# Kernel optimization log

Hardware: AMD Instinct MI355X
Metric: run time of the kernel (lower is better)

The kernel has to match this reference:

```python
import jax, jax.numpy as jnp
import numpy as np

N = 200000
E = 600000
C = 256


def setup_inputs() -> dict:
    key = jax.random.key(0)
    k1, k2, k3, k4, k5 = jax.random.split(key, 5)
    x = jax.random.normal(k1, (N, C), dtype=jnp.float32)
    sources = jax.random.randint(k2, (E,), 0, N, dtype=jnp.int64)
    targets = jax.random.randint(k3, (E,), 0, N, dtype=jnp.int64)
    norm = jax.random.uniform(k4, (N, 1), dtype=jnp.float32)
    # xavier_normal for [C, C]: std = sqrt(2 / (fan_in + fan_out))
    std = float(np.sqrt(2.0 / (C + C)))
    weight = jax.random.normal(k5, (C, C), dtype=jnp.float32) * std
    return {"x": x, "sources": sources, "targets": targets, "norm": norm, "weight": weight}


def reference(x, sources, targets, norm, weight):
    # out-of-place index_add: x + scatter_add(x[sources] -> targets)
    agg = x.at[targets].add(x[sources])  # [N, C]
    h = norm * agg                        # [N, C], norm broadcasts over channels
    return h @ weight                     # [N, C]
```

## Files before the change

kernel.cpp:

```cpp
#include <hip/hip_runtime.h>
#include <hip/hip_bf16.h>

#define NN 200000
#define NE 600000
#define CH 256
#define NBLK_SCAN 196
#define ZW_GRID 512
#define ZW_TILES 6250

typedef short bf16x8 __attribute__((ext_vector_type(8)));
typedef float f32x4 __attribute__((ext_vector_type(4)));
typedef unsigned short ushort8v __attribute__((ext_vector_type(8)));

__device__ __forceinline__ unsigned short f2bf(float f) {
    unsigned int u = __builtin_bit_cast(unsigned int, f);
    u = (u + 0x7FFFu + ((u >> 16) & 1u)) >> 16;
    return (unsigned short)u;
}
__device__ __forceinline__ float bf2f(unsigned short u) {
    unsigned int v = ((unsigned int)u) << 16;
    return __builtin_bit_cast(float, v);
}

__global__ void k_wt(const float* __restrict__ W, unsigned short* __restrict__ Wt) {
    int j = blockIdx.x, k = threadIdx.x;
    Wt[j * CH + k] = f2bf(W[k * CH + j]);
}

__global__ __launch_bounds__(256) void k_prep(const float* __restrict__ W,
                                              unsigned short* __restrict__ Wt,
                                              const int* __restrict__ te,
                                              int* __restrict__ deg) {
    const int t = blockIdx.x * 256 + threadIdx.x;
    const int S = gridDim.x * 256;
    for (int e = t; e < NE; e += S) atomicAdd(&deg[te[e]], 1);
    for (int i = t; i < CH * CH; i += S) {
        int j = i >> 8, k = i & 255;
        Wt[j * CH + k] = f2bf(W[k * CH + j]);
    }
}

__global__ __launch_bounds__(256) void k_scanA(const int* __restrict__ deg,
                                               int* __restrict__ off,
                                               int* __restrict__ bsum) {
    __shared__ int ts[256];
    int tid = threadIdx.x;
    int base = blockIdx.x * 1024 + tid * 4;
    int v[4];
#pragma unroll
    for (int j = 0; j < 4; ++j) {
        int idx = base + j;
        v[j] = (idx < NN) ? deg[idx] : 0;
    }
    int tsum = v[0] + v[1] + v[2] + v[3];
    ts[tid] = tsum;
    __syncthreads();
    int x = tsum;
    for (int ofs = 1; ofs < 256; ofs <<= 1) {
        int y = (tid >= ofs) ? ts[tid - ofs] : 0;
        __syncthreads();
        x += y;
        ts[tid] = x;
        __syncthreads();
    }
    int run = x - tsum;
#pragma unroll
    for (int j = 0; j < 4; ++j) {
        int idx = base + j;
        if (idx < NN) off[idx] = run;
        run += v[j];
    }
    if (tid == 255) bsum[blockIdx.x] = x;
}

__global__ __launch_bounds__(256) void k_scanC(int* __restrict__ off,
                                               const int* __restrict__ bsum,
                                               int* __restrict__ cur) {
    __shared__ int ts[256];
    int tid = threadIdx.x;
    int v = (tid < NBLK_SCAN) ? bsum[tid] : 0;
    ts[tid] = v;
    __syncthreads();
    int x = v;
    for (int ofs = 1; ofs < 256; ofs <<= 1) {
        int y = (tid >= ofs) ? ts[tid - ofs] : 0;
        __syncthreads();
        x += y;
        ts[tid] = x;
        __syncthreads();
    }
    const int bo = (blockIdx.x == 0) ? 0 : ts[blockIdx.x - 1];
    int base = blockIdx.x * 1024 + tid * 4;
#pragma unroll
    for (int j = 0; j < 4; ++j) {
        int idx = base + j;
        if (idx < NN) {
            int o = off[idx] + bo;
            off[idx] = o;
            cur[idx] = o;
        }
    }
}

__global__ void k_fill(const int* __restrict__ se, const int* __restrict__ te,
                       int* __restrict__ cur, int* __restrict__ elist) {
    int e = blockIdx.x * 256 + threadIdx.x;
    if (e < NE) {
        int t = te[e];
        int pos = atomicAdd(&cur[t], 1);
        elist[pos] = se[e];
    }
}

__global__ __launch_bounds__(256, 2) void k_zw(const float* __restrict__ x,
                                               const unsigned short* __restrict__ Wt,
                                               unsigned short* __restrict__ zbf,
                                               const int* __restrict__ te,
                                               int* __restrict__ deg) {
    __shared__ float lds[2][32 * CH];
    const int tid = threadIdx.x;
    const int wid = tid >> 6;
    const int lane = tid & 63;
    const int r16 = lane & 15;
    const int q = lane >> 4;

#define STAGE(buf, tile)                                                                  \
    {                                                                                     \
        const float* src = x + (size_t)(tile) * 32 * CH;                                  \
        _Pragma("unroll")                                                                 \
        for (int i = 0; i < 8; ++i) {                                                     \
            const int fi = i * 1024 + tid * 4;                                            \
            const int row = fi >> 8;                                                      \
            const int g = (fi & 255) >> 2;                                                \
            const int sg = g ^ (row & 7);                                                 \
            __builtin_amdgcn_global_load_lds(                                             \
                (const __attribute__((address_space(1))) void*)(src + row * CH + sg * 4), \
                (__attribute__((address_space(3))) void*)(&lds[buf][fi]), 16, 0, 0);      \
        }                                                                                 \
    }

    int t = blockIdx.x;
    STAGE(0, t)

    bf16x8 breg[8][4];
    {
        const unsigned short* wb = Wt + (size_t)(wid * 64 + r16) * CH + q * 8;
#pragma unroll
        for (int kk = 0; kk < 8; ++kk)
#pragma unroll
            for (int nt = 0; nt < 4; ++nt)
                breg[kk][nt] = *reinterpret_cast<const bf16x8*>(wb + (size_t)nt * 16 * CH + kk * 32);
    }

    for (int e = blockIdx.x * 256 + tid; e < NE; e += ZW_GRID * 256)
        atomicAdd(&deg[te[e]], 1);

    int cur = 0;
    for (; t < ZW_TILES; t += ZW_GRID) {
        const int tn = t + ZW_GRID;
        if (tn < ZW_TILES) STAGE(cur ^ 1, tn)
        __syncthreads();

        f32x4 acc[2][4];
#pragma unroll
        for (int m = 0; m < 2; ++m)
#pragma unroll
            for (int nt = 0; nt < 4; ++nt) acc[m][nt] = (f32x4){0.f, 0.f, 0.f, 0.f};

#pragma unroll
        for (int kk = 0; kk < 8; ++kk) {
            bf16x8 a[2];
#pragma unroll
            for (int m = 0; m < 2; ++m) {
                const int lr = m * 16 + r16;
                const int sw = lr & 7;
                const float* lp = &lds[cur][lr * CH];
                const int g0 = kk * 8 + q * 2;
                f32x4 lo = *reinterpret_cast<const f32x4*>(lp + ((g0 ^ sw) << 2));
                f32x4 hi = *reinterpret_cast<const f32x4*>(lp + (((g0 + 1) ^ sw) << 2));
                a[m][0] = (short)f2bf(lo[0]); a[m][1] = (short)f2bf(lo[1]);
                a[m][2] = (short)f2bf(lo[2]); a[m][3] = (short)f2bf(lo[3]);
                a[m][4] = (short)f2bf(hi[0]); a[m][5] = (short)f2bf(hi[1]);
                a[m][6] = (short)f2bf(hi[2]); a[m][7] = (short)f2bf(hi[3]);
            }
#pragma unroll
            for (int m = 0; m < 2; ++m)
#pragma unroll
                for (int nt = 0; nt < 4; ++nt)
                    acc[m][nt] = __builtin_amdgcn_mfma_f32_16x16x32_bf16(a[m], breg[kk][nt], acc[m][nt], 0, 0, 0);
        }

        const int rb = t * 32;
#pragma unroll
        for (int m = 0; m < 2; ++m) {
#pragma unroll
            for (int nt = 0; nt < 4; ++nt) {
                unsigned short* po = zbf + (size_t)(rb + m * 16 + q * 4) * CH
                                   + wid * 64 + nt * 16 + r16;
#pragma unroll
                for (int r = 0; r < 4; ++r) po[(size_t)r * CH] = f2bf(acc[m][nt][r]);
            }
        }
        __syncthreads();
        cur ^= 1;
    }
#undef STAGE
}

__global__ __launch_bounds__(256) void k_gout(const unsigned short* __restrict__ zbf,
                                              const int* __restrict__ off,
                                              const int* __restrict__ deg,
                                              const int* __restrict__ elist,
                                              const float* __restrict__ norm,
                                              float* __restrict__ out) {
    int wid = threadIdx.x >> 6;
    int lane = threadIdx.x & 63;
    int row = blockIdx.x * 4 + wid;
    if (row >= NN) return;
    int start = off[row];
    int d = deg[row];
    const int uo = lane * 4;
    ushort4 bv = *reinterpret_cast<const ushort4*>(zbf + (size_t)row * CH + uo);
    float ax = bf2f(bv.x), ay = bf2f(bv.y), az = bf2f(bv.z), aw = bf2f(bv.w);
    int e = 0;
    while (e < d) {
        int i0 = (e + 0 < d) ? elist[start + e + 0] : -1;
        int i1 = (e + 1 < d) ? elist[start + e + 1] : -1;
        int i2 = (e + 2 < d) ? elist[start + e + 2] : -1;
        int i3 = (e + 3 < d) ? elist[start + e + 3] : -1;
        int i4 = (e + 4 < d) ? elist[start + e + 4] : -1;
        int i5 = (e + 5 < d) ? elist[start + e + 5] : -1;
        int i6 = (e + 6 < d) ? elist[start + e + 6] : -1;
        int i7 = (e + 7 < d) ? elist[start + e + 7] : -1;
#define GACC(ii) if (ii >= 0) { \
            ushort4 v = *reinterpret_cast<const ushort4*>(zbf + (size_t)ii * CH + uo); \
            ax += bf2f(v.x); ay += bf2f(v.y); az += bf2f(v.z); aw += bf2f(v.w); }
        GACC(i0) GACC(i1) GACC(i2) GACC(i3) GACC(i4) GACC(i5) GACC(i6) GACC(i7)
#undef GACC
        e += 8;
    }
    const float nv = norm[row];
    float4 o;
    o.x = ax * nv; o.y = ay * nv; o.z = az * nv; o.w = aw * nv;
    *reinterpret_cast<float4*>(out + (size_t)row * CH + uo) = o;
}

__global__ __launch_bounds__(256, 4) void k_fgg(const float* __restrict__ x,
                                                const int* __restrict__ off,
                                                const int* __restrict__ deg,
                                                const int* __restrict__ elist,
                                                const float* __restrict__ norm,
                                                const unsigned short* __restrict__ Wt,
                                                float* __restrict__ out) {
    __shared__ unsigned short lds_a[64 * CH];
    const int tid = threadIdx.x;
    const int wid = tid >> 6;
    const int lane = tid & 63;
    const int rb = blockIdx.x * 64;
    const int rowbase = rb + wid * 16;
    const int r16 = lane & 15;
    const int q = lane >> 4;
    const int fo4 = lane * 4;

    const int offv = off[rowbase + r16];
    const int degv = deg[rowbase + r16];
    const float nv = norm[rb + lane];

    float4 acc[16];
#pragma unroll
    for (int r = 0; r < 16; ++r)
        acc[r] = *reinterpret_cast<const float4*>(x + (size_t)(rowbase + r) * CH + fo4);

#pragma unroll
    for (int r = 0; r < 16; ++r) {
        const int start = __shfl(offv, r);
        const int d = __shfl(degv, r);
        int e = 0;
        while (e < d) {
            int i0 = (e + 0 < d) ? elist[start + e + 0] : -1;
            int i1 = (e + 1 < d) ? elist[start + e + 1] : -1;
            int i2 = (e + 2 < d) ? elist[start + e + 2] : -1;
            int i3 = (e + 3 < d) ? elist[start + e + 3] : -1;
#define GACC(ii) if (ii >= 0) { \
            float4 v = *reinterpret_cast<const float4*>(x + (size_t)ii * CH + fo4); \
            acc[r].x += v.x; acc[r].y += v.y; acc[r].z += v.z; acc[r].w += v.w; }
            GACC(i0) GACC(i1) GACC(i2) GACC(i3)
#undef GACC
            e += 4;
        }
    }

    unsigned short* lb = lds_a + wid * 16 * CH;
#pragma unroll
    for (int r = 0; r < 16; ++r) {
        ushort4 w;
        w.x = f2bf(acc[r].x); w.y = f2bf(acc[r].y);
        w.z = f2bf(acc[r].z); w.w = f2bf(acc[r].w);
        const int gs = (lane >> 1) ^ (r & 7);
        *reinterpret_cast<ushort4*>(lb + r * CH + gs * 8 + (lane & 1) * 4) = w;
    }
    __syncthreads();

    f32x4 facc[4][4];
#pragma unroll
    for (int m = 0; m < 4; ++m)
#pragma unroll
        for (int nt = 0; nt < 4; ++nt) facc[m][nt] = (f32x4){0.f, 0.f, 0.f, 0.f};

    const unsigned short* wb = Wt + (size_t)(wid * 64 + r16) * CH + q * 8;

#pragma unroll
    for (int kk = 0; kk < 8; ++kk) {
        bf16x8 b[4];
#pragma unroll
        for (int nt = 0; nt < 4; ++nt)
            b[nt] = *reinterpret_cast<const bf16x8*>(wb + (size_t)nt * 16 * CH + kk * 32);
        bf16x8 a[4];
#pragma unroll
        for (int m = 0; m < 4; ++m) {
            const int lr = m * 16 + r16;
            const int idx = lr * CH + ((((kk * 4) + q) ^ (lr & 7)) << 3);
            a[m] = *reinterpret_cast<const bf16x8*>(&lds_a[idx]);
        }
#pragma unroll
        for (int m = 0; m < 4; ++m)
#pragma unroll
            for (int nt = 0; nt < 4; ++nt)
                facc[m][nt] = __builtin_amdgcn_mfma_f32_16x16x32_bf16(a[m], b[nt], facc[m][nt], 0, 0, 0);
    }

#pragma unroll
    for (int m = 0; m < 4; ++m) {
        const int crow = rb + m * 16 + q * 4;
#pragma unroll
        for (int nt = 0; nt < 4; ++nt) {
            float* po = out + (size_t)crow * CH + wid * 64 + nt * 16 + r16;
#pragma unroll
            for (int r = 0; r < 4; ++r) {
                const float nj = __shfl(nv, m * 16 + q * 4 + r);
                po[(size_t)r * CH] = facc[m][nt][r] * nj;
            }
        }
    }
}

extern "C" void kernel_launch(void* const* d_in, const int* in_sizes, int n_in,
                              void* d_out, int out_size, void* d_ws, size_t ws_size,
                              hipStream_t stream) {
    const float* x = (const float*)d_in[0];
    const int* se = (const int*)d_in[1];
    const int* te = (const int*)d_in[2];
    const float* norm = (const float*)d_in[3];
    const float* W = (const float*)d_in[4];
    float* out = (float*)d_out;

    char* ws = (char*)d_ws;
    unsigned short* Wt = (unsigned short*)ws;
    int* deg   = (int*)(ws + 131072);
    int* off   = (int*)(ws + 931072);
    int* cur   = (int*)(ws + 1731072);
    int* elist = (int*)(ws + 2531072);
    int* bsum  = (int*)(ws + 4931072);
    const size_t ZBF_OFF = 4932096;
    const size_t NEED = ZBF_OFF + (size_t)NN * CH * 2;
    const bool big = (ws_size >= NEED);
    unsigned short* zbf = (unsigned short*)(ws + ZBF_OFF);

    hipMemsetAsync(deg, 0, NN * sizeof(int), stream);
    if (big) {
        k_wt<<<CH, CH, 0, stream>>>(W, Wt);
        k_zw<<<ZW_GRID, 256, 0, stream>>>(x, Wt, zbf, te, deg);
        k_scanA<<<NBLK_SCAN, 256, 0, stream>>>(deg, off, bsum);
        k_scanC<<<NBLK_SCAN, 256, 0, stream>>>(off, bsum, cur);
        k_fill<<<(NE + 255) / 256, 256, 0, stream>>>(se, te, cur, elist);
        k_gout<<<NN / 4, 256, 0, stream>>>(zbf, off, deg, elist, norm, out);
    } else {
        k_prep<<<512, 256, 0, stream>>>(W, Wt, te, deg);
        k_scanA<<<NBLK_SCAN, 256, 0, stream>>>(deg, off, bsum);
        k_scanC<<<NBLK_SCAN, 256, 0, stream>>>(off, bsum, cur);
        k_fill<<<(NE + 255) / 256, 256, 0, stream>>>(se, te, cur, elist);
        k_fgg<<<NN / 64, 256, 0, stream>>>(x, off, deg, elist, norm, Wt, out);
    }
}
```

Before: 238.3 us.

## Prefetch x tiles through registers into single LDS buffer, reload weights per tile

```diff
diff --git a/kernel.cpp b/kernel.cpp
--- a/kernel.cpp
+++ b/kernel.cpp
@@ -117,94 +117,106 @@
                                                unsigned short* __restrict__ zbf,
                                                const int* __restrict__ te,
                                                int* __restrict__ deg) {
-    __shared__ float lds[2][32 * CH];
+    __shared__ float lds[32 * CH];
     const int tid = threadIdx.x;
     const int wid = tid >> 6;
     const int lane = tid & 63;
     const int r16 = lane & 15;
     const int q = lane >> 4;
 
-#define STAGE(buf, tile)                                                                  \
-    {                                                                                     \
-        const float* src = x + (size_t)(tile) * 32 * CH;                                  \
-        _Pragma("unroll")                                                                 \
-        for (int i = 0; i < 8; ++i) {                                                     \
-            const int fi = i * 1024 + tid * 4;                                            \
-            const int row = fi >> 8;                                                      \
-            const int g = (fi & 255) >> 2;                                                \
-            const int sg = g ^ (row & 7);                                                 \
-            __builtin_amdgcn_global_load_lds(                                             \
-                (const __attribute__((address_space(1))) void*)(src + row * CH + sg * 4), \
-                (__attribute__((address_space(3))) void*)(&lds[buf][fi]), 16, 0, 0);      \
-        }                                                                                 \
-    }
-
-    int t = blockIdx.x;
-    STAGE(0, t)
-
-    bf16x8 breg[8][4];
-    {
-        const unsigned short* wb = Wt + (size_t)(wid * 64 + r16) * CH + q * 8;
-#pragma unroll
-        for (int kk = 0; kk < 8; ++kk)
-#pragma unroll
-            for (int nt = 0; nt < 4; ++nt)
-                breg[kk][nt] = *reinterpret_cast<const bf16x8*>(wb + (size_t)nt * 16 * CH + kk * 32);
-    }
-
     for (int e = blockIdx.x * 256 + tid; e < NE; e += ZW_GRID * 256)
         atomicAdd(&deg[te[e]], 1);
 
-    int cur = 0;
+#define LOADT(st, tile)                                                            \
+    {                                                                              \
+        const float* src = x + (size_t)(tile) * 32 * CH;                           \
+        _Pragma("unroll")                                                          \
+        for (int i = 0; i < 8; ++i)                                                \
+            st[i] = *reinterpret_cast<const float4*>(src + i * 1024 + tid * 4);    \
+    }
+
+#define WRITELDS(st)                                                               \
+    {                                                                              \
+        _Pragma("unroll")                                                          \
+        for (int i = 0; i < 8; ++i) {                                              \
+            const int fi = i * 1024 + tid * 4;                                     \
+            const int row = fi >> 8;                                               \
+            const int g = (fi & 255) >> 2;                                         \
+            const int sg = g ^ (row & 7);                                          \
+            *reinterpret_cast<f32x4*>(&lds[row * CH + sg * 4]) =                   \
+                (f32x4){st[i].x, st[i].y, st[i].z, st[i].w};                       \
+        }                                                                          \
+    }
+
+#define COMPUTE(t)                                                                         \
+    {                                                                                      \
+        f32x4 acc[2][4];                                                                   \
+        _Pragma("unroll")                                                                  \
+        for (int m = 0; m < 2; ++m)                                                        \
+            for (int nt = 0; nt < 4; ++nt) acc[m][nt] = (f32x4){0.f, 0.f, 0.f, 0.f};       \
+        const unsigned short* wb = Wt + (size_t)(wid * 64 + r16) * CH + q * 8;             \
+        _Pragma("unroll")                                                                  \
+        for (int kk = 0; kk < 8; ++kk) {                                                   \
+            bf16x8 b[4];                                                                   \
+            _Pragma("unroll")                                                              \
+            for (int nt = 0; nt < 4; ++nt)                                                 \
+                b[nt] = *reinterpret_cast<const bf16x8*>(wb + (size_t)nt * 16 * CH + kk * 32); \
+            bf16x8 a[2];                                                                   \
+            _Pragma("unroll")                                                              \
+            for (int m = 0; m < 2; ++m) {                                                  \
+                const int lr = m * 16 + r16;                                               \
+                const int sw = lr & 7;                                                     \
+                const float* lp = &lds[lr * CH];                                           \
+                const int g0 = kk * 8 + q * 2;                                             \
+                f32x4 lo = *reinterpret_cast<const f32x4*>(lp + ((g0 ^ sw) << 2));         \
+                f32x4 hi = *reinterpret_cast<const f32x4*>(lp + (((g0 + 1) ^ sw) << 2));   \
+                a[m][0] = (short)f2bf(lo[0]); a[m][1] = (short)f2bf(lo[1]);                \
+                a[m][2] = (short)f2bf(lo[2]); a[m][3] = (short)f2bf(lo[3]);                \
+                a[m][4] = (short)f2bf(hi[0]); a[m][5] = (short)f2bf(hi[1]);                \
+                a[m][6] = (short)f2bf(hi[2]); a[m][7] = (short)f2bf(hi[3]);                \
+            }                                                                              \
+            _Pragma("unroll")                                                              \
+            for (int m = 0; m < 2; ++m)                                                    \
+                for (int nt = 0; nt < 4; ++nt)                                             \
+                    acc[m][nt] = __builtin_amdgcn_mfma_f32_16x16x32_bf16(a[m], b[nt], acc[m][nt], 0, 0, 0); \
+        }                                                                                  \
+        const int rb = (t) * 32;                                                           \
+        _Pragma("unroll")                                                                  \
+        for (int m = 0; m < 2; ++m) {                                                      \
+            for (int nt = 0; nt < 4; ++nt) {                                               \
+                unsigned short* po = zbf + (size_t)(rb + m * 16 + q * 4) * CH              \
+                                   + wid * 64 + nt * 16 + r16;                             \
+                _Pragma("unroll")                                                          \
+                for (int r = 0; r < 4; ++r) po[(size_t)r * CH] = f2bf(acc[m][nt][r]);      \
+            }                                                                              \
+        }                                                                                  \
+    }
+
+    float4 stA[8], stB[8];
+    int t = blockIdx.x;
+    LOADT(stA, t)
+    bool useA = true;
     for (; t < ZW_TILES; t += ZW_GRID) {
         const int tn = t + ZW_GRID;
-        if (tn < ZW_TILES) STAGE(cur ^ 1, tn)
-        __syncthreads();
-
-        f32x4 acc[2][4];
-#pragma unroll
-        for (int m = 0; m < 2; ++m)
-#pragma unroll
-            for (int nt = 0; nt < 4; ++nt) acc[m][nt] = (f32x4){0.f, 0.f, 0.f, 0.f};
-
-#pragma unroll
-        for (int kk = 0; kk < 8; ++kk) {
-            bf16x8 a[2];
-#pragma unroll
-            for (int m = 0; m < 2; ++m) {
-                const int lr = m * 16 + r16;
-                const int sw = lr & 7;
-                const float* lp = &lds[cur][lr * CH];
-                const int g0 = kk * 8 + q * 2;
-                f32x4 lo = *reinterpret_cast<const f32x4*>(lp + ((g0 ^ sw) << 2));
-                f32x4 hi = *reinterpret_cast<const f32x4*>(lp + (((g0 + 1) ^ sw) << 2));
-                a[m][0] = (short)f2bf(lo[0]); a[m][1] = (short)f2bf(lo[1]);
-                a[m][2] = (short)f2bf(lo[2]); a[m][3] = (short)f2bf(lo[3]);
-                a[m][4] = (short)f2bf(hi[0]); a[m][5] = (short)f2bf(hi[1]);
-                a[m][6] = (short)f2bf(hi[2]); a[m][7] = (short)f2bf(hi[3]);
-            }
-#pragma unroll
-            for (int m = 0; m < 2; ++m)
-#pragma unroll
-                for (int nt = 0; nt < 4; ++nt)
-                    acc[m][nt] = __builtin_amdgcn_mfma_f32_16x16x32_bf16(a[m], breg[kk][nt], acc[m][nt], 0, 0, 0);
-        }
-
-        const int rb = t * 32;
-#pragma unroll
-        for (int m = 0; m < 2; ++m) {
-#pragma unroll
-            for (int nt = 0; nt < 4; ++nt) {
-                unsigned short* po = zbf + (size_t)(rb + m * 16 + q * 4) * CH
-                                   + wid * 64 + nt * 16 + r16;
-#pragma unroll
-                for (int r = 0; r < 4; ++r) po[(size_t)r * CH] = f2bf(acc[m][nt][r]);
-            }
-        }
-        __syncthreads();
-        cur ^= 1;
-    }
-#undef STAGE
+        if (useA) {
+            if (tn < ZW_TILES) LOADT(stB, tn)
+            WRITELDS(stA)
+        } else {
+            if (tn < ZW_TILES) LOADT(stA, tn)
+            WRITELDS(stB)
+        }
+        asm volatile("s_waitcnt lgkmcnt(0)" ::: "memory");
+        __builtin_amdgcn_s_barrier();
+        __builtin_amdgcn_sched_barrier(0);
+        COMPUTE(t)
+        asm volatile("s_waitcnt lgkmcnt(0)" ::: "memory");
+        __builtin_amdgcn_s_barrier();
+        __builtin_amdgcn_sched_barrier(0);
+        useA = !useA;
+    }
+#undef LOADT
+#undef WRITELDS
+#undef COMPUTE
 }
 
 __global__ __launch_bounds__(256) void k_gout(const unsigned short* __restrict__ zbf,
```

Result: slower. 302.1 us (+26.7%).
